# Kernel optimization log

Measured on AMD Instinct MI355X. Metric: run time of the kernel, lower is better.

Reference implementation:

```python
import jax, jax.numpy as jnp
import numpy as np

B, H, L, N = 4, 256, 8192, 32  # batch, channels, seq_len, d_state//2 complex modes


def setup_inputs() -> dict:
    key = jax.random.key(0)
    ks = jax.random.split(key, 8)
    x = jax.random.normal(ks[0], (B, H, L), jnp.float32)
    # ChannelwiseLayerNorm params
    ln1_g = jnp.ones((H,), jnp.float32); ln1_b = jnp.zeros((H,), jnp.float32)
    ln2_g = jnp.ones((H,), jnp.float32); ln2_b = jnp.zeros((H,), jnp.float32)
    # S4D params (standard diagonal S4D init)
    log_dt = jax.random.uniform(ks[1], (H,), jnp.float32, np.log(1e-3), np.log(1e-1))
    log_A_real = jnp.log(0.5 * jnp.ones((H, N), jnp.float32))
    A_imag = jnp.tile(np.pi * jnp.arange(N, dtype=jnp.float32)[None, :], (H, 1))
    C_re = jax.random.normal(ks[2], (H, N), jnp.float32) * (0.5 ** 0.5)
    C_im = jax.random.normal(ks[3], (H, N), jnp.float32) * (0.5 ** 0.5)
    D = jax.random.normal(ks[4], (H,), jnp.float32)
    # 1x1 convs as dense matrices
    glu_w = jax.random.normal(ks[5], (2 * H, H), jnp.float32) * (1.0 / H) ** 0.5
    glu_b = jnp.zeros((2 * H,), jnp.float32)
    ffn_in_w = jax.random.normal(ks[6], (4 * H, H), jnp.float32) * (1.0 / H) ** 0.5
    ffn_in_b = jnp.zeros((4 * H,), jnp.float32)
    ffn_out_w = jax.random.normal(ks[7], (H, 4 * H), jnp.float32) * (1.0 / (4 * H)) ** 0.5
    ffn_out_b = jnp.zeros((H,), jnp.float32)
    return dict(x=x, ln1_g=ln1_g, ln1_b=ln1_b, ln2_g=ln2_g, ln2_b=ln2_b,
                log_dt=log_dt, log_A_real=log_A_real, A_imag=A_imag,
                C_re=C_re, C_im=C_im, D=D,
                glu_w=glu_w, glu_b=glu_b,
                ffn_in_w=ffn_in_w, ffn_in_b=ffn_in_b,
                ffn_out_w=ffn_out_w, ffn_out_b=ffn_out_b)


def _channel_ln(x, g, b, eps=1e-5):
    # normalize over channel dim (axis=1) of (B, C, L)
    mu = jnp.mean(x, axis=1, keepdims=True)
    var = jnp.var(x, axis=1, keepdims=True)
    return (x - mu) / jnp.sqrt(var + eps) * g[None, :, None] + b[None, :, None]


def _s4d(u, log_dt, log_A_real, A_imag, C_re, C_im, D):
    # u: (B, H, L); diagonal SSM via Vandermonde kernel + FFT conv
    Ls = u.shape[-1]
    dt = jnp.exp(log_dt)                       # (H,)
    A = -jnp.exp(log_A_real) + 1j * A_imag     # (H, N)
    dtA = A * dt[:, None]                      # (H, N)
    Cc = (C_re + 1j * C_im) * (jnp.exp(dtA) - 1.0) / A
    vand = jnp.exp(dtA[:, :, None] * jnp.arange(Ls))      # (H, N, L)
    K = 2.0 * jnp.einsum('hn,hnl->hl', Cc, vand).real     # (H, L)
    n = 2 * Ls
    y = jnp.fft.irfft(jnp.fft.rfft(u, n=n) * jnp.fft.rfft(K, n=n), n=n)[..., :Ls]
    return y + u * D[None, :, None]


def reference(x, ln1_g, ln1_b, ln2_g, ln2_b, log_dt, log_A_real, A_imag,
              C_re, C_im, D, glu_w, glu_b, ffn_in_w, ffn_in_b, ffn_out_w, ffn_out_b):
    # branch 1: norm -> S4D -> GELU -> 1x1 conv -> GLU -> residual
    y = _channel_ln(x, ln1_g, ln1_b)
    y = _s4d(y, log_dt, log_A_real, A_imag, C_re, C_im, D)
    y = jax.nn.gelu(y, approximate=False)
    y = jnp.einsum('oc,bcl->bol', glu_w, y) + glu_b[None, :, None]
    a, g = jnp.split(y, 2, axis=1)
    y = a * jax.nn.sigmoid(g)
    mid = x + y
    # branch 2: norm -> FFN (1x1 conv, GELU, 1x1 conv) -> residual
    y = _channel_ln(mid, ln2_g, ln2_b)
    y = jnp.einsum('oc,bcl->bol', ffn_in_w, y) + ffn_in_b[None, :, None]
    y = jax.nn.gelu(y, approximate=False)
    y = jnp.einsum('oc,bcl->bol', ffn_out_w, y) + ffn_out_b[None, :, None]
    return mid + y
```

## Files before the change

kernel.cpp:

```cpp
#include <hip/hip_runtime.h>
#include <hip/hip_bf16.h>

#define BB 4
#define HH 256
#define LL 8192
#define NN 32
#define CH 64
#define TT 128

typedef __attribute__((ext_vector_type(4))) float f32x4;
typedef __attribute__((ext_vector_type(8))) short s16x8;
typedef __attribute__((ext_vector_type(4))) short s16x4;
typedef unsigned int u32;

static __device__ __forceinline__ ushort f2bf(float f){
    union { float f; unsigned int i; } v; v.f = f;
    unsigned int x = v.i;
    return (ushort)((x + 0x7fffu + ((x >> 16) & 1u)) >> 16);
}

static __device__ __forceinline__ float fast_gelu(float x){
    float x3 = x*x*x;
    float z  = fmaf(0.03567740814f, x3, 0.7978845608f*x);
    float e  = __builtin_amdgcn_exp2f(z * 2.885390082f);
    float t  = 1.f - 2.f*__builtin_amdgcn_rcpf(e + 1.f);
    return 0.5f*x*(1.f + t);
}
static __device__ __forceinline__ float fast_sigmoid(float x){
    float e = __builtin_amdgcn_exp2f(-x * 1.442695041f);
    return __builtin_amdgcn_rcpf(1.f + e);
}

__global__ void k_prep_weights(const float* __restrict__ gw, const float* __restrict__ fiw,
                               const float* __restrict__ fow,
                               ushort* __restrict__ dglu, ushort* __restrict__ dfi,
                               ushort* __restrict__ dfo){
    int i = blockIdx.x * 256 + threadIdx.x;
    if (i < 512*256)  dglu[i] = f2bf(gw[i]);
    if (i < 1024*256) dfi[i]  = f2bf(fiw[i]);
    if (i < 1024*256) dfo[i]  = f2bf(fow[i]);
}

__global__ void k_scan_params(const float* __restrict__ log_dt, const float* __restrict__ log_A_real,
                              const float* __restrict__ A_imag, float4* __restrict__ out){
    int i = blockIdx.x * 256 + threadIdx.x;
    int h = i >> 5;
    float dt  = expf(log_dt[h]);
    float Are = -expf(log_A_real[i]);
    float Aim = A_imag[i];
    float xr = Are * dt, xi = Aim * dt;
    float er = expf(xr), sn, cs;
    sincosf(xi, &sn, &cs);
    float erT = expf(xr * (float)TT), snT, csT;
    sincosf(xi * (float)TT, &snT, &csT);
    out[i] = make_float4(er*cs, er*sn, erT*csT, erT*snT);
}

__global__ void __launch_bounds__(256) k_build(const float* __restrict__ log_dt,
      const float* __restrict__ log_A_real, const float* __restrict__ A_imag,
      const float* __restrict__ C_re, const float* __restrict__ C_im, const float* __restrict__ Dp,
      ushort* __restrict__ Tkb, ushort* __restrict__ M2b, ushort* __restrict__ V2b){
    int h = blockIdx.x, tid = threadIdx.x;
    __shared__ float prm[4][32];
    __shared__ float2 pw[129][32];
    __shared__ float kk[129];
    if (tid < 32){
        int n = tid, i = h*NN + n;
        float dt  = expf(log_dt[h]);
        float Are = -expf(log_A_real[i]);
        float Aim = A_imag[i];
        float xr = Are*dt, xi = Aim*dt;
        float er = expf(xr), sn, cs; sincosf(xi, &sn, &cs);
        float wre = er*cs, wim = er*sn;
        float nre = wre - 1.f, nim = wim;
        float inv = 1.f / (Are*Are + Aim*Aim);
        float qre = (nre*Are + nim*Aim) * inv;
        float qim = (nim*Are - nre*Aim) * inv;
        float cre = C_re[i], cim = C_im[i];
        prm[0][n] = xr; prm[1][n] = xi;
        prm[2][n] = 2.f*(cre*qre - cim*qim);
        prm[3][n] = 2.f*(cre*qim + cim*qre);
    }
    __syncthreads();
    if (tid < 129){
        float d = (float)tid, acc = 0.f;
        for (int n = 0; n < 32; ++n){
            float er = expf(prm[0][n]*d), sn, cs; sincosf(prm[1][n]*d, &sn, &cs);
            float pre = er*cs, pim = er*sn;
            pw[tid][n] = make_float2(pre, pim);
            acc += prm[2][n]*pre - prm[3][n]*pim;
        }
        kk[tid] = acc;
    }
    __syncthreads();
    float k0d = kk[0] + Dp[h];
    for (int idx = tid; idx < 128*128; idx += 256){
        int t = idx >> 7, ta = idx & 127, d = t - ta;
        float v = (d < 0) ? 0.f : ((d == 0) ? k0d : kk[d]);
        Tkb[(size_t)h*16384 + idx] = f2bf(v);
    }
    for (int idx = tid; idx < 128*64; idx += 256){
        int t = idx >> 6, j = idx & 63, n = j & 31;
        float2 p = pw[t+1][n];
        float v = (j < 32) ?  (prm[2][n]*p.x - prm[3][n]*p.y)
                           : -(prm[2][n]*p.y + prm[3][n]*p.x);
        M2b[(size_t)h*8192 + idx] = f2bf(v);
    }
    for (int idx = tid; idx < 64*128; idx += 256){
        int row = idx >> 7, ta = idx & 127, n = row & 31;
        float2 p = pw[127 - ta][n];
        V2b[(size_t)h*8192 + idx] = f2bf(row < 32 ? p.x : p.y);
    }
}

template<int MODE>
__global__ void __launch_bounds__(256) k_ln(const float* __restrict__ in, void* __restrict__ outp,
                     const float* __restrict__ gamma, const float* __restrict__ beta){
    int p = threadIdx.x & 63, cg = threadIdx.x >> 6;
    int b  = blockIdx.x / (LL/64);
    int l  = (blockIdx.x % (LL/64)) * 64 + p;
    const float* base = in + (size_t)b*HH*LL + l;
    int c0 = cg * 64;
    float s = 0.f, s2 = 0.f;
    #pragma unroll 8
    for (int j = 0; j < 64; ++j){
        float v = base[(size_t)(c0+j)*LL];
        s += v; s2 += v*v;
    }
    __shared__ float red[2][4][64];
    red[0][cg][p] = s; red[1][cg][p] = s2;
    __syncthreads();
    float ts = red[0][0][p]+red[0][1][p]+red[0][2][p]+red[0][3][p];
    float tq = red[1][0][p]+red[1][1][p]+red[1][2][p]+red[1][3][p];
    float mu   = ts * (1.f/HH);
    float var  = tq * (1.f/HH) - mu*mu;
    float rstd = rsqrtf(var + 1e-5f);
    if (MODE == 1){
        ushort* ob = (ushort*)outp + ((size_t)(b*LL + l))*HH + c0;
        #pragma unroll
        for (int j8 = 0; j8 < 8; ++j8){
            s16x8 v;
            #pragma unroll
            for (int e = 0; e < 8; ++e){
                int c = c0 + j8*8 + e;
                v[e] = (short)f2bf((base[(size_t)c*LL] - mu)*rstd*gamma[c] + beta[c]);
            }
            *(s16x8*)(ob + j8*8) = v;
        }
    } else {
        ushort* ob = (ushort*)outp + (size_t)b*HH*LL + l;
        #pragma unroll 8
        for (int j = 0; j < 64; ++j){
            int c = c0 + j;
            ob[(size_t)c*LL] = f2bf((base[(size_t)c*LL] - mu)*rstd*gamma[c] + beta[c]);
        }
    }
}

__global__ void __launch_bounds__(256) k_gemmA(const ushort* __restrict__ V2b,
                        const ushort* __restrict__ ub, float2* __restrict__ est){
    int bh = blockIdx.x, h = bh & (HH-1);
    int tid = threadIdx.x, wave = tid >> 6, lane = tid & 63;
    int m16 = lane & 15, kg = lane >> 4;
    const ushort* Vh = V2b + (size_t)h*8192;
    const ushort* ux = ub + (size_t)bh*LL;
    f32x4 acc[4] = {};
    #pragma unroll
    for (int k0 = 0; k0 < 128; k0 += 32){
        s16x8 fa = *(const s16x8*)&Vh[(wave*16 + m16)*128 + k0 + kg*8];
        #pragma unroll
        for (int nf = 0; nf < 4; ++nf){
            s16x8 fb = *(const s16x8*)&ux[(size_t)(nf*16 + m16)*128 + k0 + kg*8];
            acc[nf] = __builtin_amdgcn_mfma_f32_16x16x32_bf16(fa, fb, acc[nf], 0, 0, 0);
        }
    }
    #pragma unroll
    for (int nf = 0; nf < 4; ++nf){
        int c = nf*16 + m16;
        #pragma unroll
        for (int r = 0; r < 4; ++r){
            int srow = wave*16 + kg*4 + r;
            float* dst = (float*)&est[((size_t)bh*CH + c)*NN + (srow & 31)];
            dst[srow >> 5] = acc[nf][r];
        }
    }
}

__global__ void k_scan_B(const float4* __restrict__ par, const float2* __restrict__ est,
                         ushort* __restrict__ carr){
    int i = blockIdx.x * 256 + threadIdx.x;
    int n = i & 31, bh = i >> 5, h = bh & (HH-1);
    float4 p0 = par[h*NN + n];
    float wre = p0.z, wim = p0.w;
    float cre = 0.f, cim = 0.f;
    const float2* e = est + (size_t)bh*CH*NN + n;
    ushort* cb = carr + (size_t)bh*CH*64;
    for (int c = 0; c < CH; ++c){
        cb[c*64 + n]      = f2bf(cre);
        cb[c*64 + 32 + n] = f2bf(cim);
        float2 v = e[(size_t)c*NN];
        float nre = fmaf(wre, cre, fmaf(-wim, cim, v.x));
        float nim = fmaf(wre, cim, fmaf(wim, cre, v.y));
        cre = nre; cim = nim;
    }
}

__global__ void __launch_bounds__(256) k_gemmC(const ushort* __restrict__ Tkb,
                        const ushort* __restrict__ M2b, const ushort* __restrict__ ub,
                        const ushort* __restrict__ carr, ushort* __restrict__ gy){
    int bh = blockIdx.x, h = bh & (HH-1);
    int tid = threadIdx.x, wave = tid >> 6, lane = tid & 63;
    int m16 = lane & 15, kg = lane >> 4;
    const ushort* Th = Tkb + (size_t)h*16384;
    const ushort* Mh = M2b + (size_t)h*8192;
    const ushort* ux = ub + (size_t)bh*LL;
    const ushort* cb = carr + (size_t)bh*CH*64;
    f32x4 acc[2][4] = {};
    #pragma unroll
    for (int k0 = 0; k0 < 128; k0 += 32){
        s16x8 fa0 = *(const s16x8*)&Th[(size_t)(wave*32 + m16)*128 + k0 + kg*8];
        s16x8 fa1 = *(const s16x8*)&Th[(size_t)(wave*32 + 16 + m16)*128 + k0 + kg*8];
        #pragma unroll
        for (int nf = 0; nf < 4; ++nf){
            s16x8 fb = *(const s16x8*)&ux[(size_t)(nf*16 + m16)*128 + k0 + kg*8];
            acc[0][nf] = __builtin_amdgcn_mfma_f32_16x16x32_bf16(fa0, fb, acc[0][nf], 0, 0, 0);
            acc[1][nf] = __builtin_amdgcn_mfma_f32_16x16x32_bf16(fa1, fb, acc[1][nf], 0, 0, 0);
        }
    }
    #pragma unroll
    for (int k0 = 0; k0 < 64; k0 += 32){
        s16x8 fa0 = *(const s16x8*)&Mh[(wave*32 + m16)*64 + k0 + kg*8];
        s16x8 fa1 = *(const s16x8*)&Mh[(wave*32 + 16 + m16)*64 + k0 + kg*8];
        #pragma unroll
        for (int nf = 0; nf < 4; ++nf){
            s16x8 fb = *(const s16x8*)&cb[(nf*16 + m16)*64 + k0 + kg*8];
            acc[0][nf] = __builtin_amdgcn_mfma_f32_16x16x32_bf16(fa0, fb, acc[0][nf], 0, 0, 0);
            acc[1][nf] = __builtin_amdgcn_mfma_f32_16x16x32_bf16(fa1, fb, acc[1][nf], 0, 0, 0);
        }
    }
    #pragma unroll
    for (int mf = 0; mf < 2; ++mf){
        #pragma unroll
        for (int nf = 0; nf < 4; ++nf){
            int c = nf*16 + m16;
            int t0 = wave*32 + mf*16 + kg*4;
            s16x4 pk;
            #pragma unroll
            for (int r = 0; r < 4; ++r){
                pk[r] = (short)f2bf(fast_gelu(acc[mf][nf][r]));
            }
            *(s16x4*)&gy[(size_t)bh*LL + c*TT + t0] = pk;
        }
    }
}

__global__ void k_transpose(const ushort* __restrict__ in, ushort* __restrict__ out){
    __shared__ ushort tile[64][66];
    int tid = threadIdx.x;
    int lt = blockIdx.x, ht = blockIdx.y, b = blockIdx.z;
    const ushort* ib = in + ((size_t)b*HH + ht*64)*LL + lt*64;
    #pragma unroll
    for (int k = 0; k < 16; ++k){
        int j = tid + k*256;
        tile[j >> 6][j & 63] = ib[(size_t)(j >> 6)*LL + (j & 63)];
    }
    __syncthreads();
    ushort* obp = out + ((size_t)b*LL + lt*64)*HH + ht*64;
    #pragma unroll
    for (int k = 0; k < 16; ++k){
        int j = tid + k*256;
        obp[(size_t)(j >> 6)*HH + (j & 63)] = tile[j & 63][j >> 6];
    }
}

__global__ void __launch_bounds__(256) k_glu(const ushort* __restrict__ Wg, const ushort* __restrict__ Xt,
                     const float* __restrict__ x, const float* __restrict__ gb,
                     float* __restrict__ mid){
    int tid = threadIdx.x;
    int wave = tid >> 6, lane = tid & 63;
    int wo = wave >> 1, wl = wave & 1;
    int m16 = lane & 15, kg = lane >> 4;
    int oa = blockIdx.y * 64 + wo*32;
    int p  = blockIdx.x * 128 + wl*64;
    const ushort* xb = Xt + (size_t)p*256;
    f32x4 aa[2][4] = {}; f32x4 ag[2][4] = {};
    #pragma unroll
    for (int k0 = 0; k0 < 256; k0 += 32){
        s16x8 fba[4];
        #pragma unroll
        for (int nf = 0; nf < 4; ++nf)
            fba[nf] = *(const s16x8*)&xb[(size_t)(nf*16 + m16)*256 + k0 + kg*8];
        #pragma unroll
        for (int mf = 0; mf < 2; ++mf){
            s16x8 fa = *(const s16x8*)&Wg[(size_t)(oa + mf*16 + m16)*256 + k0 + kg*8];
            s16x8 fg = *(const s16x8*)&Wg[(size_t)(oa + 256 + mf*16 + m16)*256 + k0 + kg*8];
            #pragma unroll
            for (int nf = 0; nf < 4; ++nf){
                aa[mf][nf] = __builtin_amdgcn_mfma_f32_16x16x32_bf16(fa, fba[nf], aa[mf][nf], 0, 0, 0);
                ag[mf][nf] = __builtin_amdgcn_mfma_f32_16x16x32_bf16(fg, fba[nf], ag[mf][nf], 0, 0, 0);
            }
        }
    }
    #pragma unroll
    for (int mf = 0; mf < 2; ++mf){
        #pragma unroll
        for (int nf = 0; nf < 4; ++nf){
            int pc = p + nf*16 + m16;
            int b = pc >> 13, l = pc & (LL-1);
            #pragma unroll
            for (int r = 0; r < 4; ++r){
                int o = oa + mf*16 + kg*4 + r;
                float va  = aa[mf][nf][r] + gb[o];
                float vg  = ag[mf][nf][r] + gb[o + 256];
                float sig = fast_sigmoid(vg);
                size_t idx = ((size_t)(b*HH + o) << 13) + l;
                mid[idx] = x[idx] + va*sig;
            }
        }
    }
}

template<int KDIM, int EPI>
__global__ void __launch_bounds__(256) k_gemm_lds(const ushort* __restrict__ A,
                      const ushort* __restrict__ Bm, const float* __restrict__ bias,
                      const float* __restrict__ mid, void* __restrict__ Cout, int pbase){
    __shared__ __align__(16) ushort sh[35072];
    int tid = threadIdx.x;
    int w = tid >> 6, lane = tid & 63;
    int m16 = lane & 15, kg = lane >> 4;
    int wr = w >> 1, wc = w & 1;
    int q0  = blockIdx.x * 128;
    int oc0 = blockIdx.y * 128;
    const ushort* Arow = A  + (size_t)oc0*KDIM;
    const ushort* Brow = Bm + (size_t)q0*KDIM;
    int srow = lane >> 3, scol = (lane & 7)*8;
    f32x4 acc[4][4] = {};
    const int nK = KDIM/64;

    #define STAGE(buf, kt) { \
        int k0s = (kt)*64; \
        _Pragma("unroll") \
        for (int i = 0; i < 4; ++i){ \
            int rr = (w*4 + i)*8; \
            __builtin_amdgcn_global_load_lds( \
                (const __attribute__((address_space(1))) u32*)(Arow + (size_t)(rr + srow)*KDIM + k0s + scol), \
                (__attribute__((address_space(3))) u32*)&sh[(buf)*8192 + rr*64], 16, 0, 0); \
            __builtin_amdgcn_global_load_lds( \
                (const __attribute__((address_space(1))) u32*)(Brow + (size_t)(rr + srow)*KDIM + k0s + scol), \
                (__attribute__((address_space(3))) u32*)&sh[16384 + (buf)*8192 + rr*64], 16, 0, 0); \
        } }

    int buf = 0;
    STAGE(0, 0);
    __syncthreads();
    for (int kt = 0; kt < nK; ++kt){
        if (kt + 1 < nK) STAGE(buf^1, kt+1);
        #pragma unroll
        for (int k032 = 0; k032 < 64; k032 += 32){
            s16x8 af[4], bf[4];
            #pragma unroll
            for (int i = 0; i < 4; ++i){
                af[i] = *(const s16x8*)&sh[buf*8192 + (wr*64 + i*16 + m16)*64 + k032 + kg*8];
                bf[i] = *(const s16x8*)&sh[16384 + buf*8192 + (wc*64 + i*16 + m16)*64 + k032 + kg*8];
            }
            #pragma unroll
            for (int mf = 0; mf < 4; ++mf){
                #pragma unroll
                for (int nf = 0; nf < 4; ++nf)
                    acc[mf][nf] = __builtin_amdgcn_mfma_f32_16x16x32_bf16(af[mf], bf[nf], acc[mf][nf], 0, 0, 0);
            }
        }
        __syncthreads();
        buf ^= 1;
    }
    #undef STAGE

    if (EPI == 0){
        ushort (*lt)[136] = (ushort(*)[136])sh;
        #pragma unroll
        for (int mf = 0; mf < 4; ++mf){
            #pragma unroll
            for (int nf = 0; nf < 4; ++nf){
                int lr = wc*64 + nf*16 + m16;
                int lc = wr*64 + mf*16 + kg*4;
                s16x4 pk;
                #pragma unroll
                for (int r = 0; r < 4; ++r){
                    float v = acc[mf][nf][r] + bias[oc0 + lc + r];
                    pk[r] = (short)f2bf(fast_gelu(v));
                }
                *(s16x4*)&lt[lr][lc] = pk;
            }
        }
        __syncthreads();
        ushort* f1 = (ushort*)Cout;
        #pragma unroll
        for (int i = 0; i < 8; ++i){
            int chunk = i*256 + tid;
            int row = chunk >> 4, c16 = chunk & 15;
            s16x8 v = *(const s16x8*)&lt[row][c16*8];
            *(s16x8*)&f1[((size_t)(q0 + row) << 10) + oc0 + c16*8] = v;
        }
    } else {
        float* out = (float*)Cout;
        #pragma unroll
        for (int mf = 0; mf < 4; ++mf){
            #pragma unroll
            for (int nf = 0; nf < 4; ++nf){
                int pc = pbase + q0 + wc*64 + nf*16 + m16;
                int b = pc >> 13, l = pc & (LL-1);
                #pragma unroll
                for (int r = 0; r < 4; ++r){
                    int oc = oc0 + wr*64 + mf*16 + kg*4 + r;
                    size_t idx = ((size_t)(b*HH + oc) << 13) + l;
                    out[idx] = mid[idx] + acc[mf][nf][r] + bias[oc];
                }
            }
        }
    }
}

extern "C" void kernel_launch(void* const* d_in, const int* in_sizes, int n_in,
                              void* d_out, int out_size, void* d_ws, size_t ws_size,
                              hipStream_t stream) {
    const float* x          = (const float*)d_in[0];
    const float* ln1_g      = (const float*)d_in[1];
    const float* ln1_b      = (const float*)d_in[2];
    const float* ln2_g      = (const float*)d_in[3];
    const float* ln2_b      = (const float*)d_in[4];
    const float* log_dt     = (const float*)d_in[5];
    const float* log_A_real = (const float*)d_in[6];
    const float* A_imag     = (const float*)d_in[7];
    const float* C_re       = (const float*)d_in[8];
    const float* C_im       = (const float*)d_in[9];
    const float* Dv         = (const float*)d_in[10];
    const float* glu_w      = (const float*)d_in[11];
    const float* glu_b      = (const float*)d_in[12];
    const float* ffn_in_w   = (const float*)d_in[13];
    const float* ffn_in_b   = (const float*)d_in[14];
    const float* ffn_out_w  = (const float*)d_in[15];
    const float* ffn_out_b  = (const float*)d_in[16];
    float* out = (float*)d_out;

    char* ws = (char*)d_ws;
    const size_t MB = 1u << 20;
    float4* par  = (float4*)(ws);
    ushort* wglu = (ushort*)(ws + 256*1024);
    ushort* wfi  = (ushort*)(ws + 512*1024);
    ushort* wfo  = (ushort*)(ws + 1024*1024);
    ushort* Tkb  = (ushort*)(ws + 2*MB);
    ushort* M2b  = (ushort*)(ws + 10*MB);
    ushort* V2b  = (ushort*)(ws + 14*MB);
    ushort* ub   = (ushort*)(ws + 18*MB);
    float2* est  = (float2*)(ws + 34*MB);
    ushort* carr = (ushort*)(ws + 50*MB);
    ushort* gy   = (ushort*)(ws + 34*MB);
    ushort* gyt  = (ushort*)(ws + 50*MB);
    float*  mid  = (float*)(ws + 2*MB);
    ushort* x2t  = (ushort*)(ws + 36*MB);
    ushort* f1   = (ushort*)(ws + 52*MB);

    int G = (ws_size >= 117*MB) ? 4 : ((ws_size >= 85*MB) ? 2 : 1);

    k_prep_weights<<<1024, 256, 0, stream>>>(glu_w, ffn_in_w, ffn_out_w, wglu, wfi, wfo);
    k_scan_params<<<32, 256, 0, stream>>>(log_dt, log_A_real, A_imag, par);
    k_build<<<HH, 256, 0, stream>>>(log_dt, log_A_real, A_imag, C_re, C_im, Dv, Tkb, M2b, V2b);
    k_ln<2><<<BB*LL/64, 256, 0, stream>>>(x, ub, ln1_g, ln1_b);
    k_gemmA<<<BB*HH, 256, 0, stream>>>(V2b, ub, est);
    k_scan_B<<<BB*HH*NN/256, 256, 0, stream>>>(par, est, carr);
    k_gemmC<<<BB*HH, 256, 0, stream>>>(Tkb, M2b, ub, carr, gy);
    k_transpose<<<dim3(LL/64, HH/64, BB), 256, 0, stream>>>(gy, gyt);
    k_glu<<<dim3(BB*LL/128, 4), 256, 0, stream>>>(wglu, gyt, x, glu_b, mid);
    k_ln<1><<<BB*LL/64, 256, 0, stream>>>(mid, x2t, ln2_g, ln2_b);
    for (int b0 = 0; b0 < BB; b0 += G){
        int pbase = b0 * LL;
        k_gemm_lds<256,0><<<dim3(G*LL/128, 8), 256, 0, stream>>>(
            wfi, x2t + (size_t)pbase*256, ffn_in_b, nullptr, f1, 0);
        k_gemm_lds<1024,1><<<dim3(G*LL/128, 2), 256, 0, stream>>>(
            wfo, f1, ffn_out_b, mid, out, pbase);
    }
    (void)in_sizes; (void)n_in; (void)out_size; (void)ws_size;
}
```

Before: 334.8 us.

## Stage GLU GEMM operands through double-buffered LDS with direct global-to-LDS loads

Rewrites the GLU 1x1-conv GEMM so weight and activation tiles are loaded into shared memory via global_load_lds, double-buffered over four K-steps of 64. Waves then read MFMA fragments from LDS instead of each issuing redundant global loads. This aims to cut global memory traffic and hide load latency behind MFMAs. It uses 64 KB LDS per block, limiting occupancy. LDS rows are unpadded, which may cause bank conflicts.

```diff
diff --git a/kernel.cpp b/kernel.cpp
--- a/kernel.cpp
+++ b/kernel.cpp
@@ -276,40 +276,70 @@
 __global__ void __launch_bounds__(256) k_glu(const ushort* __restrict__ Wg, const ushort* __restrict__ Xt,
                      const float* __restrict__ x, const float* __restrict__ gb,
                      float* __restrict__ mid){
+    __shared__ __align__(16) ushort sh[32768];
     int tid = threadIdx.x;
-    int wave = tid >> 6, lane = tid & 63;
-    int wo = wave >> 1, wl = wave & 1;
+    int w = tid >> 6, lane = tid & 63;
     int m16 = lane & 15, kg = lane >> 4;
-    int oa = blockIdx.y * 64 + wo*32;
-    int p  = blockIdx.x * 128 + wl*64;
-    const ushort* xb = Xt + (size_t)p*256;
+    int wr = w >> 1, wc = w & 1;
+    int p0  = blockIdx.x * 128;
+    int oa0 = blockIdx.y * 64;
+    const ushort* Brow = Xt + (size_t)p0*256;
+    int srow = lane >> 3, scol = (lane & 7)*8;
     f32x4 aa[2][4] = {}; f32x4 ag[2][4] = {};
-    #pragma unroll
-    for (int k0 = 0; k0 < 256; k0 += 32){
-        s16x8 fba[4];
-        #pragma unroll
-        for (int nf = 0; nf < 4; ++nf)
-            fba[nf] = *(const s16x8*)&xb[(size_t)(nf*16 + m16)*256 + k0 + kg*8];
-        #pragma unroll
-        for (int mf = 0; mf < 2; ++mf){
-            s16x8 fa = *(const s16x8*)&Wg[(size_t)(oa + mf*16 + m16)*256 + k0 + kg*8];
-            s16x8 fg = *(const s16x8*)&Wg[(size_t)(oa + 256 + mf*16 + m16)*256 + k0 + kg*8];
-            #pragma unroll
-            for (int nf = 0; nf < 4; ++nf){
-                aa[mf][nf] = __builtin_amdgcn_mfma_f32_16x16x32_bf16(fa, fba[nf], aa[mf][nf], 0, 0, 0);
-                ag[mf][nf] = __builtin_amdgcn_mfma_f32_16x16x32_bf16(fg, fba[nf], ag[mf][nf], 0, 0, 0);
-            }
-        }
-    }
+
+    #define GSTAGE(buf, kt) { \
+        int k0s = (kt)*64; \
+        _Pragma("unroll") \
+        for (int i = 0; i < 4; ++i){ \
+            int rr = (w*4 + i)*8; \
+            int grow = (rr < 64) ? (oa0 + rr + srow) : (256 + oa0 + (rr - 64) + srow); \
+            __builtin_amdgcn_global_load_lds( \
+                (const __attribute__((address_space(1))) u32*)(Wg + (size_t)grow*256 + k0s + scol), \
+                (__attribute__((address_space(3))) u32*)&sh[(buf)*8192 + rr*64], 16, 0, 0); \
+            __builtin_amdgcn_global_load_lds( \
+                (const __attribute__((address_space(1))) u32*)(Brow + (size_t)(rr + srow)*256 + k0s + scol), \
+                (__attribute__((address_space(3))) u32*)&sh[16384 + (buf)*8192 + rr*64], 16, 0, 0); \
+        } }
+
+    int buf = 0;
+    GSTAGE(0, 0);
+    __syncthreads();
+    for (int kt = 0; kt < 4; ++kt){
+        if (kt + 1 < 4) GSTAGE(buf^1, kt+1);
+        #pragma unroll
+        for (int k032 = 0; k032 < 64; k032 += 32){
+            s16x8 fa[2], fg[2], fb[4];
+            #pragma unroll
+            for (int i = 0; i < 2; ++i){
+                fa[i] = *(const s16x8*)&sh[buf*8192 + (wr*32 + i*16 + m16)*64 + k032 + kg*8];
+                fg[i] = *(const s16x8*)&sh[buf*8192 + (64 + wr*32 + i*16 + m16)*64 + k032 + kg*8];
+            }
+            #pragma unroll
+            for (int i = 0; i < 4; ++i)
+                fb[i] = *(const s16x8*)&sh[16384 + buf*8192 + (wc*64 + i*16 + m16)*64 + k032 + kg*8];
+            #pragma unroll
+            for (int mf = 0; mf < 2; ++mf){
+                #pragma unroll
+                for (int nf = 0; nf < 4; ++nf){
+                    aa[mf][nf] = __builtin_amdgcn_mfma_f32_16x16x32_bf16(fa[mf], fb[nf], aa[mf][nf], 0, 0, 0);
+                    ag[mf][nf] = __builtin_amdgcn_mfma_f32_16x16x32_bf16(fg[mf], fb[nf], ag[mf][nf], 0, 0, 0);
+                }
+            }
+        }
+        __syncthreads();
+        buf ^= 1;
+    }
+    #undef GSTAGE
+
     #pragma unroll
     for (int mf = 0; mf < 2; ++mf){
         #pragma unroll
         for (int nf = 0; nf < 4; ++nf){
-            int pc = p + nf*16 + m16;
+            int pc = p0 + wc*64 + nf*16 + m16;
             int b = pc >> 13, l = pc & (LL-1);
             #pragma unroll
             for (int r = 0; r < 4; ++r){
-                int o = oa + mf*16 + kg*4 + r;
+                int o = oa0 + wr*32 + mf*16 + kg*4 + r;
                 float va  = aa[mf][nf][r] + gb[o];
                 float vg  = ag[mf][nf][r] + gb[o + 256];
                 float sig = fast_sigmoid(vg);
```

Result: faster. 305.3 us (-8.8%).
